# Kernel tuning notes

Measured on AMD Instinct MI355X. Metric: run time of the kernel, lower is better.

Reference implementation:

```python
import jax, jax.numpy as jnp
import numpy as np

N = 512          # Cartesian grid size (nRead)
C = 16           # n_coils
K = 262144       # n non-uniform k-space samples (~512 spokes x 512 readouts)


def setup_inputs() -> dict:
    key = jax.random.key(0)
    ks = jax.random.split(key, 6)
    x_real = jax.random.normal(ks[0], (C, K), jnp.float32)
    x_imag = jax.random.normal(ks[1], (C, K), jnp.float32)
    csm_real = jax.random.normal(ks[2], (C, N, N), jnp.float32)
    csm_imag = jax.random.normal(ks[3], (C, N, N), jnp.float32)
    # normalized k-space coordinates in [-0.5, 0.5)
    traj = jax.random.uniform(ks[4], (K, 2), jnp.float32, -0.5, 0.5)
    # density compensation weights (positive)
    dcf = jax.random.uniform(ks[5], (K,), jnp.float32)
    return dict(x_real=x_real, x_imag=x_imag, csm_real=csm_real,
                csm_imag=csm_imag, traj=traj, dcf=dcf)


def reference(x_real, x_imag, csm_real, csm_imag, traj, dcf):
    # Adjoint gridding NUFFT with density compensation + coil-sensitivity combine.
    # 1) density-compensate the multicoil non-Cartesian samples
    x = (x_real + 1j * x_imag) * dcf                      # [C, K] complex64
    # 2) grid (scatter-add) onto the Cartesian k-space grid (nearest-cell gridding)
    t = jax.lax.stop_gradient(traj)
    idx = jnp.round((t + 0.5) * N).astype(jnp.int32) % N  # [K, 2]
    iy, ix = idx[:, 0], idx[:, 1]
    grid = jnp.zeros((C, N, N), jnp.complex64).at[:, iy, ix].add(x)
    # 3) centered inverse FFT to image space (adjoint of DFT, scaled by N^2)
    img = jnp.fft.fftshift(
        jnp.fft.ifft2(jnp.fft.ifftshift(grid, axes=(-2, -1)), axes=(-2, -1)),
        axes=(-2, -1)) * (N * N)                          # [C, N, N]
    # 4) coil combine with conjugate sensitivity maps
    csm = csm_real + 1j * csm_imag
    out = jnp.sum(jnp.conj(csm) * img, axis=0)            # [N, N] complex64
    # return real/imag stacked, with batch dim (mimics numpy2tensor add_batch_dim)
    return jnp.stack([out.real, out.imag])[None]          # [1, 2, N, N]
```

## Files before the change

### kernel.cpp

```cpp
#include <hip/hip_runtime.h>
#include <math.h>

#define N 512
#define NN (N * N)
#define C 16
#define K 262144
#define LOG2N 9
#define NCOL 8

#define SK(e) ((e) + ((e) >> 4))
#define LROW 544


__global__ __launch_bounds__(256) void prep_hist_kernel(const float2* __restrict__ traj,
                                                        const float* __restrict__ dcf,
                                                        int* __restrict__ cell,
                                                        float* __restrict__ sdcf,
                                                        int* __restrict__ count) {
    int k = blockIdx.x * 256 + threadIdx.x;
    float2 t = traj[k];
    int iy = __float2int_rn((t.x + 0.5f) * (float)N) & (N - 1);
    int ix = __float2int_rn((t.y + 0.5f) * (float)N) & (N - 1);
    int cl = iy * N + ix;
    cell[k] = cl;
    float s = ((iy + ix) & 1) ? -1.0f : 1.0f;
    sdcf[k] = dcf[k] * s;
    atomicAdd(&count[cl], 1);
}

__global__ __launch_bounds__(256) void scan_reduce_kernel(const int* __restrict__ count,
                                                          int* __restrict__ bsum) {
    __shared__ int sd[256];
    int t = threadIdx.x;
    const int4* c4 = (const int4*)count;
    int4 v = c4[blockIdx.x * 256 + t];
    sd[t] = v.x + v.y + v.z + v.w;
    __syncthreads();
    for (int d = 128; d > 0; d >>= 1) {
        if (t < d) sd[t] += sd[t + d];
        __syncthreads();
    }
    if (t == 0) bsum[blockIdx.x] = sd[0];
}

__global__ __launch_bounds__(256) void scan_top_kernel(const int* __restrict__ bsum,
                                                       int* __restrict__ boffs,
                                                       int* __restrict__ offs) {
    __shared__ int sd[256];
    int t = threadIdx.x;
    int v = bsum[t];
    sd[t] = v;
    __syncthreads();
    for (int d = 1; d < 256; d <<= 1) {
        int tmp = (t >= d) ? sd[t - d] : 0;
        __syncthreads();
        sd[t] += tmp;
        __syncthreads();
    }
    boffs[t] = sd[t] - v;
    if (t == 0) offs[NN] = K;
}

__global__ __launch_bounds__(256) void scan_final_kernel(const int* __restrict__ count,
                                                         const int* __restrict__ boffs,
                                                         int* __restrict__ offs,
                                                         int* __restrict__ cursor) {
    __shared__ int sd[256];
    int t = threadIdx.x;
    int base_idx = blockIdx.x * 256 + t;
    const int4* c4 = (const int4*)count;
    int4 v = c4[base_idx];
    int s = v.x + v.y + v.z + v.w;
    sd[t] = s;
    __syncthreads();
    for (int d = 1; d < 256; d <<= 1) {
        int tmp = (t >= d) ? sd[t - d] : 0;
        __syncthreads();
        sd[t] += tmp;
        __syncthreads();
    }
    int base = boffs[blockIdx.x] + sd[t] - s;
    int4 o;
    o.x = base;
    o.y = base + v.x;
    o.z = base + v.x + v.y;
    o.w = base + v.x + v.y + v.z;
    ((int4*)offs)[base_idx] = o;
    ((int4*)cursor)[base_idx] = o;
}

__global__ __launch_bounds__(256) void payload_kernel(const float* __restrict__ xr,
                                                      const float* __restrict__ xi,
                                                      const int* __restrict__ cell,
                                                      const float* __restrict__ sdcf,
                                                      int* __restrict__ cursor,
                                                      float2* __restrict__ payA,
                                                      float2* __restrict__ payB) {
    __shared__ float tR[256][17];
    __shared__ float tI[256][17];
    __shared__ int   sp[256];
    __shared__ float sw[256];
    int t = threadIdx.x;
    int k0 = blockIdx.x * 256;
#pragma unroll
    for (int c = 0; c < C; ++c) {
        tR[t][c] = xr[(size_t)c * K + k0 + t];
        tI[t][c] = xi[(size_t)c * K + k0 + t];
    }
    int cl = cell[k0 + t];
    float w = sdcf[k0 + t];
    int p = atomicAdd(&cursor[cl], 1);
    sp[t] = p;
    sw[t] = w;
    __syncthreads();
    int sg = t >> 3, l = t & 7;
    for (int j = sg; j < 256; j += 32) {
        int pp = sp[j];
        float ww = sw[j];
        payA[(size_t)pp * 8 + l] = make_float2(tR[j][l] * ww,     tI[j][l] * ww);
        payB[(size_t)pp * 8 + l] = make_float2(tR[j][8 + l] * ww, tI[j][8 + l] * ww);
    }
}

__global__ __launch_bounds__(256) void build8_kernel(const int* __restrict__ offs,
                                                     const float4* __restrict__ payA4,
                                                     const float4* __restrict__ payB4,
                                                     float2* __restrict__ grid) {
    __shared__ float4 lds[4][LROW];
    int bid = blockIdx.x;
    int h = bid & 1;
    int r = bid >> 1;
    int t = threadIdx.x;
    int w = t >> 6;
    int l = t & 63;
    const float4* pay = h ? payB4 : payA4;
    const int* ro = offs + r * N;

#pragma unroll
    for (int it = 0; it < 8; ++it) {
        int col = l + (it << 6);
        int s = ro[col];
        int e = ro[col + 1];
        float4 acc = make_float4(0.f, 0.f, 0.f, 0.f);
        for (int p = s; p < e; ++p) {
            float4 v = pay[(size_t)p * 4 + w];
            acc.x += v.x; acc.y += v.y; acc.z += v.z; acc.w += v.w;
        }
        int bc = (int)(__brev((unsigned)col) >> (32 - LOG2N));
        lds[w][SK(bc)] = acc;
    }
    asm volatile("s_waitcnt lgkmcnt(0)" ::: "memory");

    for (int s = 1; s <= LOG2N; ++s) {
        int half = 1 << (s - 1);
        int m = half << 1;
#pragma unroll
        for (int i = 0; i < 4; ++i) {
            int b = l + (i << 6);
            int j = b & (half - 1);
            int grp = b >> (s - 1);
            int p1 = grp * m + j;
            int p2 = p1 + half;
            float ang = 6.283185307179586f * (float)j / (float)m;
            float sn, cs;
            __sincosf(ang, &sn, &cs);
            float4 v = lds[w][SK(p2)];
            float4 u = lds[w][SK(p1)];
            float tr0 = cs * v.x - sn * v.y;
            float ti0 = cs * v.y + sn * v.x;
            float tr1 = cs * v.z - sn * v.w;
            float ti1 = cs * v.w + sn * v.z;
            lds[w][SK(p2)] = make_float4(u.x - tr0, u.y - ti0, u.z - tr1, u.w - ti1);
            lds[w][SK(p1)] = make_float4(u.x + tr0, u.y + ti0, u.z + tr1, u.w + ti1);
        }
        asm volatile("s_waitcnt lgkmcnt(0)" ::: "memory");
    }

    int c0 = h * 8 + (w << 1);
    float2* g0 = grid + (size_t)c0 * NN + (size_t)r * N;
    float2* g1 = grid + (size_t)(c0 + 1) * NN + (size_t)r * N;
    for (int i = l; i < N; i += 64) {
        float4 v = lds[w][SK(i)];
        g0[i] = make_float2(v.x, v.y);
        g1[i] = make_float2(v.z, v.w);
    }
}

__global__ __launch_bounds__(256) void colfft_kernel(float2* __restrict__ grid) {
    __shared__ float sr[N * NCOL];
    __shared__ float si[N * NCOL];
    int blk = blockIdx.x;
    int c = blk >> 6;
    int cg = blk & 63;
    float2* base = grid + (size_t)c * NN + cg * NCOL;
    int t = threadIdx.x;

    for (int e = t; e < N * NCOL; e += 256) {
        int row = e >> 3, col = e & 7;
        float2 v = base[(size_t)row * N + col];
        sr[e] = v.x; si[e] = v.y;
    }
    __syncthreads();

    int col = t & 7;
    int tg = t >> 3;
    for (int i = tg; i < N; i += 32) {
        int j = __brev((unsigned)i) >> (32 - LOG2N);
        if (j > i) {
            int a1 = i * NCOL + col, a2 = j * NCOL + col;
            float a = sr[a1]; sr[a1] = sr[a2]; sr[a2] = a;
            float b = si[a1]; si[a1] = si[a2]; si[a2] = b;
        }
    }
    __syncthreads();

    for (int s = 1; s <= LOG2N; ++s) {
        int half = 1 << (s - 1);
        int m = half << 1;
        for (int b = tg; b < 256; b += 32) {
            int j = b & (half - 1);
            int grp = b >> (s - 1);
            int p1 = grp * m + j;
            int p2 = p1 + half;
            float ang = 6.283185307179586f * (float)j / (float)m;
            float sn, cs;
            __sincosf(ang, &sn, &cs);
            int a1 = p1 * NCOL + col, a2 = p2 * NCOL + col;
            float xr2 = sr[a2], xi2 = si[a2];
            float tr = cs * xr2 - sn * xi2;
            float ti = cs * xi2 + sn * xr2;
            float ur = sr[a1], ui = si[a1];
            sr[a2] = ur - tr; si[a2] = ui - ti;
            sr[a1] = ur + tr; si[a1] = ui + ti;
        }
        __syncthreads();
    }

    for (int e = t; e < N * NCOL; e += 256) {
        int row = e >> 3, col2 = e & 7;
        base[(size_t)row * N + col2] = make_float2(sr[e], si[e]);
    }
}

__global__ __launch_bounds__(256) void combine_kernel(const float* __restrict__ csr,
                                                      const float* __restrict__ csi,
                                                      const float2* __restrict__ grid,
                                                      float* __restrict__ out) {
    int pix = blockIdx.x * 256 + threadIdx.x;
    int ny = pix >> LOG2N, nx = pix & (N - 1);
    float ar = 0.f, ai = 0.f;
#pragma unroll
    for (int c = 0; c < C; ++c) {
        float2 uv = grid[(size_t)c * NN + pix];
        float a = csr[c * NN + pix];
        float b = csi[c * NN + pix];
        ar += a * uv.x + b * uv.y;
        ai += a * uv.y - b * uv.x;
    }
    float s = ((ny + nx) & 1) ? -1.f : 1.f;
    out[pix] = s * ar;
    out[NN + pix] = s * ai;
}

extern "C" void kernel_launch(void* const* d_in, const int* in_sizes, int n_in,
                              void* d_out, int out_size, void* d_ws, size_t ws_size,
                              hipStream_t stream) {
    const float* x_real   = (const float*)d_in[0];
    const float* x_imag   = (const float*)d_in[1];
    const float* csm_real = (const float*)d_in[2];
    const float* csm_imag = (const float*)d_in[3];
    const float2* traj    = (const float2*)d_in[4];
    const float* dcf      = (const float*)d_in[5];
    float* out = (float*)d_out;

    char* ws = (char*)d_ws;
    size_t o = 0;
    float* grid  = (float*)(ws + o); o += (size_t)C * NN * 2 * sizeof(float);
    int*   cell  = (int*)(ws + o);   o += (size_t)K * sizeof(int);
    float* sdcf  = (float*)(ws + o); o += (size_t)K * sizeof(float);
    int*   count = (int*)(ws + o);   o += (size_t)NN * sizeof(int);
    int*   offs  = (int*)(ws + o);   o += ((size_t)NN + 4) * sizeof(int);
    int*   cursor= (int*)(ws + o);   o += (size_t)NN * sizeof(int);
    float2* payA = (float2*)(ws + o); o += (size_t)K * 8 * sizeof(float2);
    float2* payB = (float2*)(ws + o); o += (size_t)K * 8 * sizeof(float2);
    int*   bsum  = (int*)(ws + o);   o += 256 * sizeof(int);
    int*   boffs = (int*)(ws + o);   o += 256 * sizeof(int);

    (void)hipMemsetAsync(count, 0, (size_t)NN * sizeof(int), stream);

    prep_hist_kernel<<<K / 256, 256, 0, stream>>>(traj, dcf, cell, sdcf, count);
    scan_reduce_kernel<<<256, 256, 0, stream>>>(count, bsum);
    scan_top_kernel<<<1, 256, 0, stream>>>(bsum, boffs, offs);
    scan_final_kernel<<<256, 256, 0, stream>>>(count, boffs, offs, cursor);
    payload_kernel<<<K / 256, 256, 0, stream>>>(x_real, x_imag, cell, sdcf, cursor, payA, payB);
    build8_kernel<<<N * 2, 256, 0, stream>>>(offs, (const float4*)payA, (const float4*)payB, (float2*)grid);
    colfft_kernel<<<C * (N / NCOL), 256, 0, stream>>>((float2*)grid);
    combine_kernel<<<NN / 256, 256, 0, stream>>>(csm_real, csm_imag, (float2*)grid, out);
}
```

Measured before the change: 215.9 us.

## Unify payload buffer, prefetch first samples, rewrite column FFT with per-wave float4 butterflies

The two half-coil payload buffers are merged into one interleaved 16-coil buffer, so each sample writes one contiguous 128-byte line. The row-build kernel now loads all segment bounds and the first payload element for its 8 columns up front to raise memory-level parallelism. The column FFT is rewritten to match the row FFT: each wave owns two columns as float4 in skewed LDS, does the bit-reversal during the load, and replaces block barriers with wave-local waitcnt. The risks are wider strided float4 column loads and higher register pressure from the prefetch arrays.

Measured after the change: 211.4 us. 1.02x faster.

```diff
diff --git a/kernel.cpp b/kernel.cpp
--- a/kernel.cpp
+++ b/kernel.cpp
@@ -6,7 +6,6 @@
 #define C 16
 #define K 262144
 #define LOG2N 9
-#define NCOL 8
 
 #define SK(e) ((e) + ((e) >> 4))
 #define LROW 544
@@ -94,8 +93,7 @@
                                                       const int* __restrict__ cell,
                                                       const float* __restrict__ sdcf,
                                                       int* __restrict__ cursor,
-                                                      float2* __restrict__ payA,
-                                                      float2* __restrict__ payB) {
+                                                      float2* __restrict__ pay) {
     __shared__ float tR[256][17];
     __shared__ float tI[256][17];
     __shared__ int   sp[256];
@@ -109,22 +107,19 @@
     }
     int cl = cell[k0 + t];
     float w = sdcf[k0 + t];
-    int p = atomicAdd(&cursor[cl], 1);
-    sp[t] = p;
+    sp[t] = atomicAdd(&cursor[cl], 1);
     sw[t] = w;
     __syncthreads();
-    int sg = t >> 3, l = t & 7;
-    for (int j = sg; j < 256; j += 32) {
+    int sg = t >> 4, l = t & 15;
+    for (int j = sg; j < 256; j += 16) {
         int pp = sp[j];
         float ww = sw[j];
-        payA[(size_t)pp * 8 + l] = make_float2(tR[j][l] * ww,     tI[j][l] * ww);
-        payB[(size_t)pp * 8 + l] = make_float2(tR[j][8 + l] * ww, tI[j][8 + l] * ww);
+        pay[(size_t)pp * 16 + l] = make_float2(tR[j][l] * ww, tI[j][l] * ww);
     }
 }
 
 __global__ __launch_bounds__(256) void build8_kernel(const int* __restrict__ offs,
-                                                     const float4* __restrict__ payA4,
-                                                     const float4* __restrict__ payB4,
+                                                     const float4* __restrict__ pay4,
                                                      float2* __restrict__ grid) {
     __shared__ float4 lds[4][LROW];
     int bid = blockIdx.x;
@@ -133,19 +128,30 @@
     int t = threadIdx.x;
     int w = t >> 6;
     int l = t & 63;
-    const float4* pay = h ? payB4 : payA4;
+    int q = h * 4 + w;
     const int* ro = offs + r * N;
 
+    int sv[8], ev[8];
 #pragma unroll
     for (int it = 0; it < 8; ++it) {
         int col = l + (it << 6);
-        int s = ro[col];
-        int e = ro[col + 1];
-        float4 acc = make_float4(0.f, 0.f, 0.f, 0.f);
-        for (int p = s; p < e; ++p) {
-            float4 v = pay[(size_t)p * 4 + w];
-            acc.x += v.x; acc.y += v.y; acc.z += v.z; acc.w += v.w;
+        sv[it] = ro[col];
+        ev[it] = ro[col + 1];
+    }
+    float4 vv[8];
+#pragma unroll
+    for (int it = 0; it < 8; ++it) {
+        vv[it] = make_float4(0.f, 0.f, 0.f, 0.f);
+        if (sv[it] < ev[it]) vv[it] = pay4[(size_t)sv[it] * 8 + q];
+    }
+#pragma unroll
+    for (int it = 0; it < 8; ++it) {
+        float4 acc = vv[it];
+        for (int p = sv[it] + 1; p < ev[it]; ++p) {
+            float4 v2 = pay4[(size_t)p * 8 + q];
+            acc.x += v2.x; acc.y += v2.y; acc.z += v2.z; acc.w += v2.w;
         }
+        int col = l + (it << 6);
         int bc = (int)(__brev((unsigned)col) >> (32 - LOG2N));
         lds[w][SK(bc)] = acc;
     }
@@ -156,9 +162,9 @@
         int m = half << 1;
 #pragma unroll
         for (int i = 0; i < 4; ++i) {
-            int b = l + (i << 6);
-            int j = b & (half - 1);
-            int grp = b >> (s - 1);
+            int b2 = l + (i << 6);
+            int j = b2 & (half - 1);
+            int grp = b2 >> (s - 1);
             int p1 = grp * m + j;
             int p2 = p1 + half;
             float ang = 6.283185307179586f * (float)j / (float)m;
@@ -176,7 +182,7 @@
         asm volatile("s_waitcnt lgkmcnt(0)" ::: "memory");
     }
 
-    int c0 = h * 8 + (w << 1);
+    int c0 = q * 2;
     float2* g0 = grid + (size_t)c0 * NN + (size_t)r * N;
     float2* g1 = grid + (size_t)(c0 + 1) * NN + (size_t)r * N;
     for (int i = l; i < N; i += 64) {
@@ -187,58 +193,54 @@
 }
 
 __global__ __launch_bounds__(256) void colfft_kernel(float2* __restrict__ grid) {
-    __shared__ float sr[N * NCOL];
-    __shared__ float si[N * NCOL];
+    __shared__ float4 lds[4][LROW];
     int blk = blockIdx.x;
     int c = blk >> 6;
     int cg = blk & 63;
-    float2* base = grid + (size_t)c * NN + cg * NCOL;
-    int t = threadIdx.x;
-
-    for (int e = t; e < N * NCOL; e += 256) {
-        int row = e >> 3, col = e & 7;
-        float2 v = base[(size_t)row * N + col];
-        sr[e] = v.x; si[e] = v.y;
-    }
-    __syncthreads();
-
-    int col = t & 7;
-    int tg = t >> 3;
-    for (int i = tg; i < N; i += 32) {
-        int j = __brev((unsigned)i) >> (32 - LOG2N);
-        if (j > i) {
-            int a1 = i * NCOL + col, a2 = j * NCOL + col;
-            float a = sr[a1]; sr[a1] = sr[a2]; sr[a2] = a;
-            float b = si[a1]; si[a1] = si[a2]; si[a2] = b;
-        }
-    }
-    __syncthreads();
+    int t = threadIdx.x;
+    int w = t >> 6;
+    int l = t & 63;
+    int colb = cg * 8 + w * 2;
+    float2* gp = grid + (size_t)c * NN + colb;
+
+#pragma unroll
+    for (int j = 0; j < 8; ++j) {
+        int row = l + (j << 6);
+        float4 v = *(const float4*)(gp + (size_t)row * N);
+        int br = (int)(__brev((unsigned)row) >> (32 - LOG2N));
+        lds[w][SK(br)] = v;
+    }
+    asm volatile("s_waitcnt lgkmcnt(0)" ::: "memory");
 
     for (int s = 1; s <= LOG2N; ++s) {
         int half = 1 << (s - 1);
         int m = half << 1;
-        for (int b = tg; b < 256; b += 32) {
-            int j = b & (half - 1);
-            int grp = b >> (s - 1);
+#pragma unroll
+        for (int i = 0; i < 4; ++i) {
+            int b2 = l + (i << 6);
+            int j = b2 & (half - 1);
+            int grp = b2 >> (s - 1);
             int p1 = grp * m + j;
             int p2 = p1 + half;
             float ang = 6.283185307179586f * (float)j / (float)m;
             float sn, cs;
             __sincosf(ang, &sn, &cs);
-            int a1 = p1 * NCOL + col, a2 = p2 * NCOL + col;
-            float xr2 = sr[a2], xi2 = si[a2];
-            float tr = cs * xr2 - sn * xi2;
-            float ti = cs * xi2 + sn * xr2;
-            float ur = sr[a1], ui = si[a1];
-            sr[a2] = ur - tr; si[a2] = ui - ti;
-            sr[a1] = ur + tr; si[a1] = ui + ti;
+            float4 v = lds[w][SK(p2)];
+            float4 u = lds[w][SK(p1)];
+            float tr0 = cs * v.x - sn * v.y;
+            float ti0 = cs * v.y + sn * v.x;
+            float tr1 = cs * v.z - sn * v.w;
+            float ti1 = cs * v.w + sn * v.z;
+            lds[w][SK(p2)] = make_float4(u.x - tr0, u.y - ti0, u.z - tr1, u.w - ti1);
+            lds[w][SK(p1)] = make_float4(u.x + tr0, u.y + ti0, u.z + tr1, u.w + ti1);
         }
-        __syncthreads();
-    }
-
-    for (int e = t; e < N * NCOL; e += 256) {
-        int row = e >> 3, col2 = e & 7;
-        base[(size_t)row * N + col2] = make_float2(sr[e], si[e]);
+        asm volatile("s_waitcnt lgkmcnt(0)" ::: "memory");
+    }
+
+#pragma unroll
+    for (int j = 0; j < 8; ++j) {
+        int i = l + (j << 6);
+        *(float4*)(gp + (size_t)i * N) = lds[w][SK(i)];
     }
 }
 
@@ -281,8 +283,7 @@
     int*   count = (int*)(ws + o);   o += (size_t)NN * sizeof(int);
     int*   offs  = (int*)(ws + o);   o += ((size_t)NN + 4) * sizeof(int);
     int*   cursor= (int*)(ws + o);   o += (size_t)NN * sizeof(int);
-    float2* payA = (float2*)(ws + o); o += (size_t)K * 8 * sizeof(float2);
-    float2* payB = (float2*)(ws + o); o += (size_t)K * 8 * sizeof(float2);
+    float2* pay  = (float2*)(ws + o); o += (size_t)K * 16 * sizeof(float2);
     int*   bsum  = (int*)(ws + o);   o += 256 * sizeof(int);
     int*   boffs = (int*)(ws + o);   o += 256 * sizeof(int);
 
@@ -292,8 +293,8 @@
     scan_reduce_kernel<<<256, 256, 0, stream>>>(count, bsum);
     scan_top_kernel<<<1, 256, 0, stream>>>(bsum, boffs, offs);
     scan_final_kernel<<<256, 256, 0, stream>>>(count, boffs, offs, cursor);
-    payload_kernel<<<K / 256, 256, 0, stream>>>(x_real, x_imag, cell, sdcf, cursor, payA, payB);
-    build8_kernel<<<N * 2, 256, 0, stream>>>(offs, (const float4*)payA, (const float4*)payB, (float2*)grid);
-    colfft_kernel<<<C * (N / NCOL), 256, 0, stream>>>((float2*)grid);
+    payload_kernel<<<K / 256, 256, 0, stream>>>(x_real, x_imag, cell, sdcf, cursor, pay);
+    build8_kernel<<<N * 2, 256, 0, stream>>>(offs, (const float4*)pay, (float2*)grid);
+    colfft_kernel<<<C * 64, 256, 0, stream>>>((float2*)grid);
     combine_kernel<<<NN / 256, 256, 0, stream>>>(csm_real, csm_imag, (float2*)grid, out);
 }
```
